# Kernel optimization log

Measured on AMD Instinct MI355X. Metric: run time of the kernel, lower is better.

The kernel has to match this reference:

```python
import jax, jax.numpy as jnp
import numpy as np

B, R, L, D, F = 64, 50, 15, 1024, 4096  # batch, num_boxes, max_phrase_len, pooling_dim, densecap_feat_dim


def setup_inputs() -> dict:
    key = jax.random.key(0)
    k1, k2, k3, k4 = jax.random.split(key, 4)
    features = jax.random.normal(k1, (B, R, F), dtype=jnp.float32)
    # zero-padded phrase token embeddings per region
    phrase_lengths = jax.random.randint(k2, (B, R), 1, L + 1, dtype=jnp.int32)
    phrases = jax.random.normal(k3, (B, R, L, D), dtype=jnp.float32)
    tok_mask = (jnp.arange(L)[None, None, :] < phrase_lengths[:, :, None]).astype(jnp.float32)
    phrases = phrases * tok_mask[..., None]  # zero padding beyond each phrase length
    # image_pass Linear params (xavier_uniform weight, zero bias)
    limit = float(np.sqrt(6.0 / (F + D)))
    W = jax.random.uniform(k4, (D, F), dtype=jnp.float32, minval=-limit, maxval=limit)
    b = jnp.zeros((D,), dtype=jnp.float32)
    return {"features": features, "phrases": phrases, "W": W, "b": b,
            "phrase_lengths": phrase_lengths}


def reference(features, phrases, W, b, phrase_lengths):
    # segment-mean over phrase tokens: sum of zero-padded tokens / true length
    mean_phrase = jnp.sum(phrases, axis=2) / phrase_lengths[:, :, None].astype(phrases.dtype)  # [B,R,D]
    vis = jax.nn.relu(jnp.einsum('brf,df->brd', features, W) + b)  # [B,R,D]
    return jnp.concatenate([vis, mean_phrase], axis=2)  # [B,R,2D]
```

## Files before the change

kernel.cpp:

```cpp
#include <hip/hip_runtime.h>

#define NB   64
#define NR   50
#define LTOK 15
#define DIM  1024
#define FEAT 4096
#define MTOT (NB*NR)
#define OSTRIDE (2*DIM)

typedef __attribute__((ext_vector_type(8))) short bf16x8;
typedef __attribute__((ext_vector_type(4))) float f32x4;

#define WS_AH 0ull
#define WS_AL 26214400ull
#define WS_BH 52428800ull
#define WS_BL 60817408ull
#define WS_PB 69206016ull
#define WS_NEED 121634816ull

#define NSPLIT 4
#define KSTEPS_TOTAL 384
#define KS_PER_SPLIT 96
#define GEMM_BLOCKS 800

#define GLOAD16(gsrc, ldst)                                                   \
    __builtin_amdgcn_global_load_lds(                                         \
        (__attribute__((address_space(1))) void*)(gsrc),                      \
        (__attribute__((address_space(3))) void*)(ldst), 16, 0, 0)

__device__ __forceinline__ void split_trunc(float x, unsigned short& h, unsigned short& l) {
    unsigned int u = __builtin_bit_cast(unsigned int, x);
    h = (unsigned short)(u >> 16);
    float r = x - __builtin_bit_cast(float, u & 0xffff0000u);
    l = (unsigned short)(__builtin_bit_cast(unsigned int, r) >> 16);
}

__global__ __launch_bounds__(256) void split_kernel(
    const float* __restrict__ A, const float* __restrict__ W,
    unsigned short* __restrict__ Ah, unsigned short* __restrict__ Al,
    unsigned short* __restrict__ Bh, unsigned short* __restrict__ Bl)
{
    const int NA4 = MTOT * FEAT / 4;
    const int NW4 = DIM * FEAT / 4;
    for (int i = blockIdx.x * 256 + threadIdx.x; i < NA4 + NW4;
         i += gridDim.x * 256) {
        const bool isA = i < NA4;
        const int  j   = isA ? i : i - NA4;
        const float4 v = isA ? reinterpret_cast<const float4*>(A)[j]
                             : reinterpret_cast<const float4*>(W)[j];
        ushort4 h, l;
        split_trunc(v.x, h.x, l.x); split_trunc(v.y, h.y, l.y);
        split_trunc(v.z, h.z, l.z); split_trunc(v.w, h.w, l.w);
        if (isA) {
            reinterpret_cast<ushort4*>(Ah)[j] = h;
            reinterpret_cast<ushort4*>(Al)[j] = l;
        } else {
            reinterpret_cast<ushort4*>(Bh)[j] = h;
            reinterpret_cast<ushort4*>(Bl)[j] = l;
        }
    }
}

__global__ __launch_bounds__(256, 3) void gemm_mp_kernel(
    const unsigned short* __restrict__ Ah, const unsigned short* __restrict__ Al,
    const unsigned short* __restrict__ Bh, const unsigned short* __restrict__ Bl,
    const float* __restrict__ phrases, const int* __restrict__ lengths,
    float* __restrict__ pbuf, float* __restrict__ out)
{
    if (blockIdx.x >= GEMM_BLOCKS) {
        const int br = blockIdx.x - GEMM_BLOCKS;
        const int d4 = threadIdx.x;
        const float4* p = reinterpret_cast<const float4*>(
            phrases + (size_t)br * LTOK * DIM) + d4;
        float4 acc = make_float4(0.f, 0.f, 0.f, 0.f);
        #pragma unroll
        for (int l = 0; l < LTOK; ++l) {
            float4 v = p[(size_t)l * (DIM / 4)];
            acc.x += v.x; acc.y += v.y; acc.z += v.z; acc.w += v.w;
        }
        const float inv = 1.0f / (float)lengths[br];
        acc.x *= inv; acc.y *= inv; acc.z *= inv; acc.w *= inv;
        reinterpret_cast<float4*>(out + (size_t)br * OSTRIDE + DIM)[d4] = acc;
        return;
    }

    __shared__ unsigned short At[2][128][32];
    __shared__ unsigned short Bt[2][128][32];

    const int bid  = blockIdx.x;
    const int nt   = bid & 7;
    const int rest = bid >> 3;
    const int mt   = rest % 25;
    const int q    = rest / 25;

    const int tid  = threadIdx.x;
    const int lane = tid & 63;
    const int w    = tid >> 6;
    const int wr   = (w >> 1) * 64;
    const int wc   = (w & 1) * 64;
    const int fr   = lane & 15;
    const int fk   = (lane >> 4) * 8;

    const int c0    = w * 2;
    const int srow  = lane >> 2;
    const int skoff = (lane & 3) * 8;
    const unsigned aoff0 = (unsigned)(mt * 128 + 16 * c0      + srow) * FEAT + skoff;
    const unsigned aoff1 = (unsigned)(mt * 128 + 16 * (c0+1)  + srow) * FEAT + skoff;
    const unsigned boff0 = (unsigned)(nt * 128 + 16 * c0      + srow) * FEAT + skoff;
    const unsigned boff1 = (unsigned)(nt * 128 + 16 * (c0+1)  + srow) * FEAT + skoff;

    auto stage = [&](int buf, int s) {
        const unsigned short* aS = (s < 128) ? Ah : (s < 256 ? Al : Ah);
        const unsigned short* bS = (s < 256) ? Bh : Bl;
        const unsigned kk = (unsigned)(s & 127) * 32;
        GLOAD16(aS + aoff0 + kk, &At[buf][16 * c0][0]);
        GLOAD16(aS + aoff1 + kk, &At[buf][16 * c0 + 16][0]);
        GLOAD16(bS + boff0 + kk, &Bt[buf][16 * c0][0]);
        GLOAD16(bS + boff1 + kk, &Bt[buf][16 * c0 + 16][0]);
    };

    f32x4 acc[4][4] = {};
    const int s0 = q * KS_PER_SPLIT;

    stage(0, s0);
    __syncthreads();

    for (int i = 0; i < KS_PER_SPLIT; ++i) {
        const int buf = i & 1;
        if (i + 1 < KS_PER_SPLIT) stage(buf ^ 1, s0 + i + 1);

        bf16x8 a[4], b[4];
        #pragma unroll
        for (int m = 0; m < 4; ++m)
            a[m] = *reinterpret_cast<const bf16x8*>(&At[buf][wr + m * 16 + fr][fk]);
        #pragma unroll
        for (int n = 0; n < 4; ++n)
            b[n] = *reinterpret_cast<const bf16x8*>(&Bt[buf][wc + n * 16 + fr][fk]);

        #pragma unroll
        for (int m = 0; m < 4; ++m)
            #pragma unroll
            for (int n = 0; n < 4; ++n)
                acc[m][n] = __builtin_amdgcn_mfma_f32_16x16x32_bf16(
                    a[m], b[n], acc[m][n], 0, 0, 0);

        __syncthreads();
    }

    const int prow0 = mt * 128 + wr + (lane >> 4) * 4;
    const int pcol0 = nt * 128 + wc + fr;
    float* pq = pbuf + (size_t)q * MTOT * DIM;
    #pragma unroll
    for (int m = 0; m < 4; ++m)
        #pragma unroll
        for (int n = 0; n < 4; ++n)
            #pragma unroll
            for (int r = 0; r < 4; ++r)
                pq[(size_t)(prow0 + m * 16 + r) * DIM + (pcol0 + n * 16)] =
                    acc[m][n][r];
}

__global__ __launch_bounds__(256) void epi_kernel(
    const float* __restrict__ pbuf, const float* __restrict__ bias,
    float* __restrict__ out)
{
    const int r = blockIdx.x;
    const int j = threadIdx.x;
    const size_t qs = (size_t)MTOT * (DIM / 4);
    const float4* p = reinterpret_cast<const float4*>(pbuf) + (size_t)r * (DIM / 4) + j;
    float4 s0 = p[0], s1 = p[qs], s2 = p[2 * qs], s3 = p[3 * qs];
    const float4 bv = reinterpret_cast<const float4*>(bias)[j];
    float4 v;
    v.x = fmaxf(s0.x + s1.x + s2.x + s3.x + bv.x, 0.f);
    v.y = fmaxf(s0.y + s1.y + s2.y + s3.y + bv.y, 0.f);
    v.z = fmaxf(s0.z + s1.z + s2.z + s3.z + bv.z, 0.f);
    v.w = fmaxf(s0.w + s1.w + s2.w + s3.w + bv.w, 0.f);
    reinterpret_cast<float4*>(out + (size_t)r * OSTRIDE)[j] = v;
}

__global__ __launch_bounds__(256) void mean_pool_kernel(
    const float* __restrict__ phrases, const int* __restrict__ lengths,
    float* __restrict__ out)
{
    const int br = blockIdx.x;
    const int d4 = threadIdx.x;
    const float4* p = reinterpret_cast<const float4*>(
        phrases + (size_t)br * LTOK * DIM) + d4;
    float4 acc = make_float4(0.f, 0.f, 0.f, 0.f);
    #pragma unroll
    for (int l = 0; l < LTOK; ++l) {
        float4 v = p[(size_t)l * (DIM / 4)];
        acc.x += v.x; acc.y += v.y; acc.z += v.z; acc.w += v.w;
    }
    const float inv = 1.0f / (float)lengths[br];
    acc.x *= inv; acc.y *= inv; acc.z *= inv; acc.w *= inv;
    reinterpret_cast<float4*>(out + (size_t)br * OSTRIDE + DIM)[d4] = acc;
}

#define BM 128
#define BN 128
#define BK 32
#define LDSP 40

__device__ __forceinline__ unsigned short bf16_rne(float f) {
    unsigned int u = __builtin_bit_cast(unsigned int, f);
    unsigned int r = (u + 0x7fffu + ((u >> 16) & 1u)) >> 16;
    return (unsigned short)r;
}
__device__ __forceinline__ float bf16_to_f(unsigned short h) {
    return __builtin_bit_cast(float, (unsigned int)h << 16);
}
__device__ __forceinline__ void split4(const float4 v, ushort4& h, ushort4& l) {
    h.x = bf16_rne(v.x); l.x = bf16_rne(v.x - bf16_to_f(h.x));
    h.y = bf16_rne(v.y); l.y = bf16_rne(v.y - bf16_to_f(h.y));
    h.z = bf16_rne(v.z); l.z = bf16_rne(v.z - bf16_to_f(h.z));
    h.w = bf16_rne(v.w); l.w = bf16_rne(v.w - bf16_to_f(h.w));
}

__global__ __launch_bounds__(256, 1) void gemm_relu_mfma(
    const float* __restrict__ A, const float* __restrict__ Bw,
    const float* __restrict__ bias, float* __restrict__ out)
{
    __shared__ __align__(16) unsigned short AhS[BM][LDSP];
    __shared__ __align__(16) unsigned short AlS[BM][LDSP];
    __shared__ __align__(16) unsigned short BhS[BN][LDSP];
    __shared__ __align__(16) unsigned short BlS[BN][LDSP];

    const int tid = threadIdx.x;
    const int m0  = blockIdx.y * BM;
    const int n0  = blockIdx.x * BN;
    const int srow = tid >> 3;
    const int scol = (tid & 7) * 4;
    const float* Aptr = A  + (size_t)(m0 + srow) * FEAT + scol;
    const float* Bptr = Bw + (size_t)(n0 + srow) * FEAT + scol;
    const int lane = tid & 63;
    const int wr   = ((tid >> 6) >> 1) * 64;
    const int wc   = ((tid >> 6) & 1) * 64;
    const int fr   = lane & 15;
    const int fk   = (lane >> 4) * 8;

    f32x4 acc[4][4] = {};
    float4 pa[4], pb[4];
    #pragma unroll
    for (int p = 0; p < 4; ++p) {
        pa[p] = *reinterpret_cast<const float4*>(Aptr + (size_t)(p * 32) * FEAT);
        pb[p] = *reinterpret_cast<const float4*>(Bptr + (size_t)(p * 32) * FEAT);
    }
    const int NK = FEAT / BK;
    for (int kt = 0; kt < NK; ++kt) {
        __syncthreads();
        #pragma unroll
        for (int p = 0; p < 4; ++p) {
            const int r = srow + p * 32;
            ushort4 h, l;
            split4(pa[p], h, l);
            *reinterpret_cast<ushort4*>(&AhS[r][scol]) = h;
            *reinterpret_cast<ushort4*>(&AlS[r][scol]) = l;
            split4(pb[p], h, l);
            *reinterpret_cast<ushort4*>(&BhS[r][scol]) = h;
            *reinterpret_cast<ushort4*>(&BlS[r][scol]) = l;
        }
        __syncthreads();
        if (kt + 1 < NK) {
            const float* An = Aptr + (size_t)(kt + 1) * BK;
            const float* Bn = Bptr + (size_t)(kt + 1) * BK;
            #pragma unroll
            for (int p = 0; p < 4; ++p) {
                pa[p] = *reinterpret_cast<const float4*>(An + (size_t)(p * 32) * FEAT);
                pb[p] = *reinterpret_cast<const float4*>(Bn + (size_t)(p * 32) * FEAT);
            }
        }
        bf16x8 fah[4], fal[4], fbh[4], fbl[4];
        #pragma unroll
        for (int m = 0; m < 4; ++m) {
            fah[m] = *reinterpret_cast<const bf16x8*>(&AhS[wr + m * 16 + fr][fk]);
            fal[m] = *reinterpret_cast<const bf16x8*>(&AlS[wr + m * 16 + fr][fk]);
        }
        #pragma unroll
        for (int n = 0; n < 4; ++n) {
            fbh[n] = *reinterpret_cast<const bf16x8*>(&BhS[wc + n * 16 + fr][fk]);
            fbl[n] = *reinterpret_cast<const bf16x8*>(&BlS[wc + n * 16 + fr][fk]);
        }
        #pragma unroll
        for (int m = 0; m < 4; ++m)
            #pragma unroll
            for (int n = 0; n < 4; ++n) {
                acc[m][n] = __builtin_amdgcn_mfma_f32_16x16x32_bf16(fah[m], fbl[n], acc[m][n], 0, 0, 0);
                acc[m][n] = __builtin_amdgcn_mfma_f32_16x16x32_bf16(fal[m], fbh[n], acc[m][n], 0, 0, 0);
                acc[m][n] = __builtin_amdgcn_mfma_f32_16x16x32_bf16(fah[m], fbh[n], acc[m][n], 0, 0, 0);
            }
    }
    const int orow0 = m0 + wr + (lane >> 4) * 4;
    const int ocol0 = n0 + wc + fr;
    #pragma unroll
    for (int n = 0; n < 4; ++n) {
        const float bv = bias[ocol0 + n * 16];
        #pragma unroll
        for (int m = 0; m < 4; ++m)
            #pragma unroll
            for (int r = 0; r < 4; ++r) {
                float v = acc[m][n][r] + bv;
                out[(size_t)(orow0 + m * 16 + r) * OSTRIDE + (ocol0 + n * 16)] =
                    fmaxf(v, 0.f);
            }
    }
}

extern "C" void kernel_launch(void* const* d_in, const int* in_sizes, int n_in,
                              void* d_out, int out_size, void* d_ws, size_t ws_size,
                              hipStream_t stream) {
    const float* features = (const float*)d_in[0];
    const float* phrases  = (const float*)d_in[1];
    const float* W        = (const float*)d_in[2];
    const float* bias     = (const float*)d_in[3];
    const int*   lengths  = (const int*)d_in[4];
    float* out = (float*)d_out;

    if (ws_size >= WS_NEED) {
        char* ws = (char*)d_ws;
        unsigned short* Ah = (unsigned short*)(ws + WS_AH);
        unsigned short* Al = (unsigned short*)(ws + WS_AL);
        unsigned short* Bh = (unsigned short*)(ws + WS_BH);
        unsigned short* Bl = (unsigned short*)(ws + WS_BL);
        float* pbuf = (float*)(ws + WS_PB);

        split_kernel<<<dim3(2048), dim3(256), 0, stream>>>(
            features, W, Ah, Al, Bh, Bl);
        gemm_mp_kernel<<<dim3(GEMM_BLOCKS + MTOT), dim3(256), 0, stream>>>(
            Ah, Al, Bh, Bl, phrases, lengths, pbuf, out);
        epi_kernel<<<dim3(MTOT), dim3(256), 0, stream>>>(pbuf, bias, out);
    } else {
        mean_pool_kernel<<<dim3(MTOT), dim3(256), 0, stream>>>(phrases, lengths, out);
        gemm_relu_mfma<<<dim3(DIM / BN, MTOT / BM), dim3(256), 0, stream>>>(
            features, W, bias, out);
    }
}
```

Measured before the change: 428.8 us.

## Triple-buffer GEMM K loop, interleave mean-pool blocks, skip padded phrase tokens

The split-K GEMM moves from double to triple LDS buffering. It waits with s_waitcnt vmcnt plus a single barrier per K-step, replacing two __syncthreads, so global-to-LDS loads run two stages ahead of the MFMAs. Mean-pool blocks are interleaved with GEMM blocks (four of every five) and the GEMM tile mapping is remapped into groups, spreading memory-bound work alongside compute-bound work. The mean-pool loop now reads only the valid tokens of each phrase rather than all fifteen. The cost is more LDS per block, which may reduce occupancy, plus a few harmless prefetch loads past the end of each split.

```diff
diff --git a/kernel.cpp b/kernel.cpp
--- a/kernel.cpp
+++ b/kernel.cpp
@@ -18,10 +18,8 @@
 #define WS_PB 69206016ull
 #define WS_NEED 121634816ull
 
-#define NSPLIT 4
-#define KSTEPS_TOTAL 384
 #define KS_PER_SPLIT 96
-#define GEMM_BLOCKS 800
+#define TOTAL_BLOCKS 4160
 
 #define GLOAD16(gsrc, ldst)                                                   \
     __builtin_amdgcn_global_load_lds(                                         \
@@ -67,31 +65,38 @@
     const float* __restrict__ phrases, const int* __restrict__ lengths,
     float* __restrict__ pbuf, float* __restrict__ out)
 {
-    if (blockIdx.x >= GEMM_BLOCKS) {
-        const int br = blockIdx.x - GEMM_BLOCKS;
-        const int d4 = threadIdx.x;
+    const int bid = blockIdx.x;
+
+    if (bid % 5 != 0) {
+        const int br = bid - bid / 5 - 1;
+        if (br >= MTOT) return;
+        const int len = lengths[br];
+        const int d4  = threadIdx.x;
         const float4* p = reinterpret_cast<const float4*>(
             phrases + (size_t)br * LTOK * DIM) + d4;
         float4 acc = make_float4(0.f, 0.f, 0.f, 0.f);
-        #pragma unroll
-        for (int l = 0; l < LTOK; ++l) {
+        #pragma unroll 3
+        for (int l = 0; l < len; ++l) {
             float4 v = p[(size_t)l * (DIM / 4)];
             acc.x += v.x; acc.y += v.y; acc.z += v.z; acc.w += v.w;
         }
-        const float inv = 1.0f / (float)lengths[br];
+        const float inv = 1.0f / (float)len;
         acc.x *= inv; acc.y *= inv; acc.z *= inv; acc.w *= inv;
         reinterpret_cast<float4*>(out + (size_t)br * OSTRIDE + DIM)[d4] = acc;
         return;
     }
 
-    __shared__ unsigned short At[2][128][32];
-    __shared__ unsigned short Bt[2][128][32];
-
-    const int bid  = blockIdx.x;
-    const int nt   = bid & 7;
-    const int rest = bid >> 3;
-    const int mt   = rest % 25;
-    const int q    = rest / 25;
+    const int g   = bid / 5;
+    const int s8  = g >> 6;
+    const int rem = g & 63;
+    const int nt  = rem >> 3;
+    const int G   = s8 * 8 + (rem & 7);
+    if (G >= 100) return;
+    const int q   = G / 25;
+    const int mt  = G % 25;
+
+    __shared__ unsigned short At[3][128][32];
+    __shared__ unsigned short Bt[3][128][32];
 
     const int tid  = threadIdx.x;
     const int lane = tid & 63;
@@ -123,12 +128,15 @@
     const int s0 = q * KS_PER_SPLIT;
 
     stage(0, s0);
-    __syncthreads();
+    stage(1, s0 + 1);
 
     for (int i = 0; i < KS_PER_SPLIT; ++i) {
-        const int buf = i & 1;
-        if (i + 1 < KS_PER_SPLIT) stage(buf ^ 1, s0 + i + 1);
-
+        asm volatile("s_waitcnt vmcnt(4)" ::: "memory");
+        __builtin_amdgcn_s_barrier();
+
+        stage((i + 2) % 3, s0 + i + 2);
+
+        const int buf = i % 3;
         bf16x8 a[4], b[4];
         #pragma unroll
         for (int m = 0; m < 4; ++m)
@@ -143,9 +151,9 @@
             for (int n = 0; n < 4; ++n)
                 acc[m][n] = __builtin_amdgcn_mfma_f32_16x16x32_bf16(
                     a[m], b[n], acc[m][n], 0, 0, 0);
-
-        __syncthreads();
-    }
+    }
+
+    asm volatile("s_waitcnt vmcnt(0)" ::: "memory");
 
     const int prow0 = mt * 128 + wr + (lane >> 4) * 4;
     const int pcol0 = nt * 128 + wc + fr;
@@ -326,7 +334,7 @@
 
         split_kernel<<<dim3(2048), dim3(256), 0, stream>>>(
             features, W, Ah, Al, Bh, Bl);
-        gemm_mp_kernel<<<dim3(GEMM_BLOCKS + MTOT), dim3(256), 0, stream>>>(
+        gemm_mp_kernel<<<dim3(TOTAL_BLOCKS), dim3(256), 0, stream>>>(
             Ah, Al, Bh, Bl, phrases, lengths, pbuf, out);
         epi_kernel<<<dim3(MTOT), dim3(256), 0, stream>>>(pbuf, bias, out);
     } else {
```

Measured after the change: 450.0 us. +5.0%, slower.
